# Kernel optimization log

Hardware: AMD Instinct MI355X
Metric: run time of the kernel (lower is better)

## Reference

```python
import jax, jax.numpy as jnp
import numpy as np

D_MODEL = 1024
N_HEADS = 16
HEAD_DIM = 64
T = 4096
ROT = HEAD_DIM // 2          # 32 channels get rotary
PAIR = ROT // 2              # 16 cos/sin frequencies
EPS = 1e-6
SCALE = 0.12                 # constant attention scale (not 1/sqrt(d))
ROPE_BASE = 10000.0
VOCAB = 50257


def setup_inputs() -> dict:
    key = jax.random.key(0)
    k_x, k_qkv, k_o, k_tok = jax.random.split(key, 4)
    bound = 0.5 / np.sqrt(D_MODEL)
    x = jax.random.normal(k_x, (1, T, D_MODEL), dtype=jnp.float32)
    w_qkv = jax.random.uniform(k_qkv, (3 * D_MODEL, D_MODEL), jnp.float32, -bound, bound)
    # module uses zero_init for w_o; use small random so output is non-trivial
    w_o = jax.random.uniform(k_o, (D_MODEL, D_MODEL), jnp.float32, -bound, bound)
    q_norm_w = jnp.ones((HEAD_DIM,), jnp.float32)
    k_norm_w = jnp.ones((HEAD_DIM,), jnp.float32)
    tokens = jax.random.randint(k_tok, (1, T), 0, VOCAB, dtype=jnp.int64)
    pos = jnp.arange(T, dtype=jnp.int64)
    # RotaryCache: inv_freq over pair dims, cos/sin of t * inv_freq
    inv_freq = 1.0 / (ROPE_BASE ** (jnp.arange(PAIR, dtype=jnp.float32) / PAIR))
    freqs = jnp.arange(T, dtype=jnp.float32)[:, None] * inv_freq[None, :]  # [T, PAIR]
    return {
        "x": x, "tokens": tokens, "pos": pos,
        "w_qkv": w_qkv, "w_o": w_o,
        "q_norm_w": q_norm_w, "k_norm_w": k_norm_w,
        "cos": jnp.cos(freqs), "sin": jnp.sin(freqs),
        "window_tokens": 1024, "block_size": 128,
    }


def _rmsnorm(x, w):
    var = jnp.mean(x * x, axis=-1, keepdims=True)
    return x * jax.lax.rsqrt(var + EPS) * w


def reference(x, tokens, pos, w_qkv, w_o, q_norm_w, k_norm_w, cos, sin,
              window_tokens, block_size):
    B, Tq, C = x.shape
    H, Dh = N_HEADS, HEAD_DIM
    qkv = x @ w_qkv.T                                  # [B, T, 3C]
    q, k, v = jnp.split(qkv, 3, axis=-1)

    def to_bhtd(t):
        return t.reshape(B, Tq, H, Dh).transpose(0, 2, 1, 3)
    q, k, v = to_bhtd(q), to_bhtd(k), to_bhtd(v)

    q = _rmsnorm(q, q_norm_w)
    k = _rmsnorm(k, k_norm_w)

    # half-truncated RoPE: rotate first ROT channels pairwise (even/odd)
    c = cos[pos][None, None]                           # [1,1,T,PAIR]
    s = sin[pos][None, None]

    def rope_rotate(t):
        t1, t2 = t[..., :ROT], t[..., ROT:]
        even, odd = t1[..., 0::2], t1[..., 1::2]
        r_even = even * c - odd * s
        r_odd = even * s + odd * c
        t1r = jnp.stack([r_even, r_odd], axis=-1).reshape(t1.shape)
        return jnp.concatenate([t1r, t2], axis=-1)

    q = rope_rotate(q)
    k = rope_rotate(k)

    v = v * 0.5                                        # no value-embed branch

    scores = jnp.einsum('bhtd,bhsd->bhts', q, k) * SCALE
    idx = jnp.arange(Tq)
    diff = idx[:, None] - idx[None, :]
    allowed = (diff >= 0) & (diff < window_tokens)     # sliding causal window
    scores = jnp.where(allowed, scores, -jnp.inf)
    p = jax.nn.softmax(scores, axis=-1)
    out = jnp.einsum('bhts,bhsd->bhtd', p, v)
    out = out.transpose(0, 2, 1, 3).reshape(B, Tq, C)
    return out @ w_o.T
```

## Files before the change

### kernel.cpp

```cpp
#include <hip/hip_runtime.h>


typedef __bf16 bf16x8 __attribute__((ext_vector_type(8)));
typedef __bf16 bf16x2 __attribute__((ext_vector_type(2)));
typedef float f32x4 __attribute__((ext_vector_type(4)));
typedef unsigned short u16x8 __attribute__((ext_vector_type(8)));
typedef unsigned short u16x4 __attribute__((ext_vector_type(4)));

#define MFMA16(a, b, c) __builtin_amdgcn_mfma_f32_16x16x32_bf16((a), (b), (c), 0, 0, 0)

__device__ __forceinline__ unsigned short f2bf(float f) {
    unsigned int u = __float_as_uint(f);
    u += 0x7fffu + ((u >> 16) & 1u);
    return (unsigned short)(u >> 16);
}
__device__ __forceinline__ float bf2f(unsigned short h) {
    return __uint_as_float(((unsigned int)h) << 16);
}
__device__ __forceinline__ unsigned int pk2bf(float a, float b) {
#if __has_builtin(__builtin_amdgcn_cvt_pk_bf16_f32)
    bf16x2 v = __builtin_amdgcn_cvt_pk_bf16_f32(a, b);
    return __builtin_bit_cast(unsigned int, v);
#else
    return (unsigned int)f2bf(a) | ((unsigned int)f2bf(b) << 16);
#endif
}
__device__ __forceinline__ float fexp2(float x) {
#if __has_builtin(__builtin_amdgcn_exp2f)
    return __builtin_amdgcn_exp2f(x);
#else
    return exp2f(x);
#endif
}

__device__ __forceinline__ void gl_lds16(const void* g, void* l) {
    typedef __attribute__((address_space(1))) unsigned int GU;
    typedef __attribute__((address_space(3))) unsigned int LU;
    __builtin_amdgcn_global_load_lds((GU*)(unsigned long long)g,
                                     (LU*)(unsigned int)(unsigned long long)l,
                                     16, 0, 0);
}

__global__ void cvt3_kernel(const float* __restrict__ x,
                            const float* __restrict__ wqkv,
                            const float* __restrict__ wo,
                            unsigned short* __restrict__ xb,
                            unsigned short* __restrict__ wqkvb,
                            unsigned short* __restrict__ wob) {
    int i = blockIdx.x * 256 + threadIdx.x;
    const float* src;
    unsigned short* dst;
    int off;
    if (i < 1048576) { src = x; dst = xb; off = i; }
    else if (i < 1835008) { src = wqkv; dst = wqkvb; off = i - 1048576; }
    else { src = wo; dst = wob; off = i - 1835008; }
    float4 f = ((const float4*)src)[off];
    u16x4 o;
    o[0] = f2bf(f.x); o[1] = f2bf(f.y); o[2] = f2bf(f.z); o[3] = f2bf(f.w);
    ((u16x4*)dst)[off] = o;
}

#define TBS 72
__global__ __launch_bounds__(256, 6) void gemm_qkv(
    const unsigned short* __restrict__ A,
    const unsigned short* __restrict__ Bt,
    const float* __restrict__ cosb, const float* __restrict__ sinb,
    const float* __restrict__ qw, const float* __restrict__ kw,
    unsigned short* __restrict__ Qb,
    unsigned short* __restrict__ Kb,
    unsigned short* __restrict__ Vt)
{
    __shared__ unsigned short smem[12288];
    unsigned short* As0 = smem;
    unsigned short* As1 = smem + 2048;
    unsigned short* Bs0 = smem + 4096;
    unsigned short* Bs1 = smem + 8192;

    const int tid = threadIdx.x;
    const int wave = tid >> 6, lane = tid & 63;
    const int quad = lane >> 4, l16 = lane & 15;
    const int m0 = blockIdx.x * 64, n0 = blockIdx.y * 128;
    const int wm = (wave >> 1) * 32, wn = (wave & 1) * 64;

    f32x4 acc[2][4];
#pragma unroll
    for (int i = 0; i < 2; ++i)
#pragma unroll
        for (int j = 0; j < 4; ++j) acc[i][j] = (f32x4){0.f, 0.f, 0.f, 0.f};

    const int lrow = lane >> 2, lcol = (lane & 3) * 8;

    for (int k0 = 0; k0 < 1024; k0 += 64) {
        {
            const unsigned short* ab = A + (size_t)(m0 + wave * 16 + lrow) * 1024 + k0 + lcol;
            gl_lds16(ab,      &As0[wave * 512]);
            gl_lds16(ab + 32, &As1[wave * 512]);
        }
#pragma unroll
        for (int i = 0; i < 2; ++i) {
            const int c = wave * 2 + i;
            const unsigned short* bb = Bt + (size_t)(n0 + c * 16 + lrow) * 1024 + k0 + lcol;
            gl_lds16(bb,      &Bs0[c * 512]);
            gl_lds16(bb + 32, &Bs1[c * 512]);
        }
        __syncthreads();
        {
            bf16x8 af[2], bfr[4];
#pragma unroll
            for (int mt = 0; mt < 2; ++mt)
                af[mt] = *(const bf16x8*)&As0[(wm + mt * 16 + l16) * 32 + quad * 8];
#pragma unroll
            for (int nt = 0; nt < 4; ++nt)
                bfr[nt] = *(const bf16x8*)&Bs0[(wn + nt * 16 + l16) * 32 + quad * 8];
#pragma unroll
            for (int mt = 0; mt < 2; ++mt)
#pragma unroll
                for (int nt = 0; nt < 4; ++nt)
                    acc[mt][nt] = MFMA16(af[mt], bfr[nt], acc[mt][nt]);
        }
        {
            bf16x8 af[2], bfr[4];
#pragma unroll
            for (int mt = 0; mt < 2; ++mt)
                af[mt] = *(const bf16x8*)&As1[(wm + mt * 16 + l16) * 32 + quad * 8];
#pragma unroll
            for (int nt = 0; nt < 4; ++nt)
                bfr[nt] = *(const bf16x8*)&Bs1[(wn + nt * 16 + l16) * 32 + quad * 8];
#pragma unroll
            for (int mt = 0; mt < 2; ++mt)
#pragma unroll
                for (int nt = 0; nt < 4; ++nt)
                    acc[mt][nt] = MFMA16(af[mt], bfr[nt], acc[mt][nt]);
        }
        __syncthreads();
    }

    unsigned short* tbw = smem + wave * 1152;
    const int region = blockIdx.y >> 3;
    const int h = ((blockIdx.y & 7) << 1) + (wave & 1);

    if (region < 2) {
        const float* wgt = region ? kw : qw;
        unsigned short* dst = region ? Kb : Qb;
        const float post = region ? 1.f : 0.17312340490667046f;
        float w[4];
#pragma unroll
        for (int nt = 0; nt < 4; ++nt) w[nt] = wgt[nt * 16 + l16] * post;
#pragma unroll
        for (int mt = 0; mt < 2; ++mt) {
#pragma unroll
            for (int r = 0; r < 4; ++r) {
                const int row = m0 + wm + mt * 16 + quad * 4 + r;
                float ss = 0.f;
#pragma unroll
                for (int nt = 0; nt < 4; ++nt)
                    ss += acc[mt][nt][r] * acc[mt][nt][r];
                ss += __shfl_xor(ss, 1); ss += __shfl_xor(ss, 2);
                ss += __shfl_xor(ss, 4); ss += __shfl_xor(ss, 8);
                const float rn = rsqrtf(ss * (1.f / 64.f) + 1e-6f);
                float val[4];
#pragma unroll
                for (int nt = 0; nt < 4; ++nt)
                    val[nt] = acc[mt][nt][r] * rn * w[nt];
#pragma unroll
                for (int nt = 0; nt < 2; ++nt) {
                    const float prt = __shfl_xor(val[nt], 1);
                    const int p = nt * 8 + (l16 >> 1);
                    const float c = cosb[row * 16 + p];
                    const float s = sinb[row * 16 + p];
                    val[nt] = (l16 & 1) ? (prt * s + val[nt] * c)
                                        : (val[nt] * c - prt * s);
                }
#pragma unroll
                for (int nt = 0; nt < 4; ++nt)
                    tbw[(quad * 4 + r) * TBS + nt * 16 + l16] = f2bf(val[nt]);
            }
            const int t = lane >> 2, dcol = (lane & 3) * 16;
            u16x8 v0 = *(const u16x8*)&tbw[t * TBS + dcol];
            u16x8 v1 = *(const u16x8*)&tbw[t * TBS + dcol + 8];
            const size_t ob = ((size_t)h * 4096 + (m0 + wm + mt * 16 + t)) * 64 + dcol;
            *(u16x8*)&dst[ob] = v0;
            *(u16x8*)&dst[ob + 8] = v1;
        }
    } else {
#pragma unroll
        for (int mt = 0; mt < 2; ++mt) {
#pragma unroll
            for (int nt = 0; nt < 4; ++nt)
#pragma unroll
                for (int r = 0; r < 4; ++r)
                    tbw[(nt * 16 + l16) * 16 + quad * 4 + r] =
                        f2bf(acc[mt][nt][r] * 0.5f);
            u16x8 v0 = *(const u16x8*)&tbw[lane * 16];
            u16x8 v1 = *(const u16x8*)&tbw[lane * 16 + 8];
            const size_t vo = ((size_t)h * 64 + lane) * 4096 + m0 + wm + mt * 16;
            *(u16x8*)&Vt[vo] = v0;
            *(u16x8*)&Vt[vo + 8] = v1;
        }
    }
}

#define PSTR 72

template <int MODE>
__device__ __forceinline__ void attn_step(
    int s0, int tq, int wave, int quad, int l16, int krow, int kcol,
    const unsigned short* __restrict__ Kh, const unsigned short* __restrict__ Vh,
    unsigned short* Ks0, unsigned short* Ks1,
    unsigned short* Vs0, unsigned short* Vs1, unsigned short* Pw,
    const bf16x8 qf0, const bf16x8 qf1, f32x4 (&o)[4], float& lsum)
{
    __syncthreads();
    const unsigned short* kb = Kh + (size_t)(s0 + krow) * 64 + kcol;
    const unsigned short* vb = Vh + (size_t)krow * 4096 + s0 + kcol;
    gl_lds16(kb,      &Ks0[wave * 512]);
    gl_lds16(kb + 32, &Ks1[wave * 512]);
    gl_lds16(vb,      &Vs0[wave * 512]);
    gl_lds16(vb + 32, &Vs1[wave * 512]);
    __syncthreads();

#pragma unroll
    for (int i = 0; i < 4; ++i) {
        const bf16x8 kf0 = *(const bf16x8*)&Ks0[(i * 16 + l16) * 32 + quad * 8];
        const bf16x8 kf1 = *(const bf16x8*)&Ks1[(i * 16 + l16) * 32 + quad * 8];
        f32x4 z = (f32x4){0.f, 0.f, 0.f, 0.f};
        z = MFMA16(kf0, qf0, z);
        z = MFMA16(kf1, qf1, z);
        float p[4];
#pragma unroll
        for (int r = 0; r < 4; ++r) {
            float e = fexp2(z[r]);
            if (MODE == 1) {
                const int s = s0 + i * 16 + quad * 4 + r;
                e = ((tq - s) < 1024) ? e : 0.f;
            }
            if (MODE == 2) {
                const int s = s0 + i * 16 + quad * 4 + r;
                e = (s <= tq) ? e : 0.f;
            }
            p[r] = e;
            lsum += e;
        }
        uint2 pk;
        pk.x = pk2bf(p[0], p[1]);
        pk.y = pk2bf(p[2], p[3]);
        *(uint2*)&Pw[l16 * PSTR + i * 16 + quad * 4] = pk;
    }
    const bf16x8 pf0 = *(const bf16x8*)&Pw[l16 * PSTR + quad * 8];
    const bf16x8 pf1 = *(const bf16x8*)&Pw[l16 * PSTR + 32 + quad * 8];
#pragma unroll
    for (int dt = 0; dt < 4; ++dt) {
        const bf16x8 vf0 = *(const bf16x8*)&Vs0[(dt * 16 + l16) * 32 + quad * 8];
        const bf16x8 vf1 = *(const bf16x8*)&Vs1[(dt * 16 + l16) * 32 + quad * 8];
        o[dt] = MFMA16(pf0, vf0, o[dt]);
        o[dt] = MFMA16(pf1, vf1, o[dt]);
    }
}

__global__ __launch_bounds__(256) void attn_kernel(
    const unsigned short* __restrict__ Qb,
    const unsigned short* __restrict__ Kb,
    const unsigned short* __restrict__ Vt,
    unsigned short* __restrict__ att)
{
    __shared__ unsigned short Ks0[64 * 32];
    __shared__ unsigned short Ks1[64 * 32];
    __shared__ unsigned short Vs0[64 * 32];
    __shared__ unsigned short Vs1[64 * 32];
    __shared__ unsigned short P[4][16 * PSTR];

    const int bid = blockIdx.x;
    const int h = ((bid & 7) << 1) | ((bid >> 3) & 1);
    const int t0 = (63 - (bid >> 4)) * 64;

    const int tid = threadIdx.x;
    const int wave = tid >> 6, lane = tid & 63;
    const int quad = lane >> 4, l16 = lane & 15;
    const int qt0 = t0 + wave * 16;
    const int tq = qt0 + l16;
    const int krow = tid >> 2, kcol = (tid & 3) * 8;

    const unsigned short* Qh = Qb + (size_t)h * 4096 * 64;
    const unsigned short* Kh = Kb + (size_t)h * 4096 * 64;
    const unsigned short* Vh = Vt + (size_t)h * 64 * 4096;

    const bf16x8 qf0 = *(const bf16x8*)&Qh[(qt0 + l16) * 64 + quad * 8];
    const bf16x8 qf1 = *(const bf16x8*)&Qh[(qt0 + l16) * 64 + 32 + quad * 8];

    f32x4 o[4];
#pragma unroll
    for (int dt = 0; dt < 4; ++dt) o[dt] = (f32x4){0.f, 0.f, 0.f, 0.f};
    float lsum = 0.f;
    unsigned short* Pw = P[wave];

    int s0 = (t0 >= 1024) ? (t0 - 1024) : 0;
    if (t0 >= 1024) {
        attn_step<1>(s0, tq, wave, quad, l16, krow, kcol, Kh, Vh,
                     Ks0, Ks1, Vs0, Vs1, Pw, qf0, qf1, o, lsum);
        s0 += 64;
    }
    for (; s0 < t0; s0 += 64)
        attn_step<0>(s0, tq, wave, quad, l16, krow, kcol, Kh, Vh,
                     Ks0, Ks1, Vs0, Vs1, Pw, qf0, qf1, o, lsum);
    attn_step<2>(t0, tq, wave, quad, l16, krow, kcol, Kh, Vh,
                 Ks0, Ks1, Vs0, Vs1, Pw, qf0, qf1, o, lsum);

    lsum += __shfl_xor(lsum, 16);
    lsum += __shfl_xor(lsum, 32);
    float lr[4];
#pragma unroll
    for (int r = 0; r < 4; ++r) lr[r] = 1.f / __shfl(lsum, quad * 4 + r);
#pragma unroll
    for (int dt = 0; dt < 4; ++dt)
#pragma unroll
        for (int r = 0; r < 4; ++r)
            att[(size_t)(qt0 + quad * 4 + r) * 1024 + h * 64 + dt * 16 + l16] =
                f2bf(o[dt][r] * lr[r]);
}

template <int BM, bool F32OUT>
__global__ __launch_bounds__(256) void gemm_bt(
    const unsigned short* __restrict__ A,
    const unsigned short* __restrict__ Bt,
    void* __restrict__ Cp, int N, int K) {
    __shared__ unsigned short As[2][BM * 32];
    __shared__ unsigned short Bs[2][128 * 32];
    constexpr int MT = BM / 32;
    const int tid = threadIdx.x;
    const int wave = tid >> 6, lane = tid & 63;
    const int quad = lane >> 4, l16 = lane & 15;
    const int m0 = blockIdx.x * BM, n0 = blockIdx.y * 128;
    const int wm = (wave >> 1) * (BM / 2), wn = (wave & 1) * 64;

    f32x4 acc[MT][4];
#pragma unroll
    for (int i = 0; i < MT; ++i)
#pragma unroll
        for (int j = 0; j < 4; ++j) acc[i][j] = (f32x4){0.f, 0.f, 0.f, 0.f};

    auto stageAB = [&](int buf, int k0) {
#pragma unroll
        for (int i = 0; i < BM / 64; ++i) {
            const int c = wave * (BM / 64) + i;
            const int e = (c * 64 + lane) * 8;
            const int r = e >> 5, col = e & 31;
            gl_lds16(A + (size_t)(m0 + r) * K + (k0 + col), &As[buf][c * 512]);
        }
#pragma unroll
        for (int i = 0; i < 2; ++i) {
            const int c = wave * 2 + i;
            const int e = (c * 64 + lane) * 8;
            const int r = e >> 5, col = e & 31;
            gl_lds16(Bt + (size_t)(n0 + r) * K + (k0 + col), &Bs[buf][c * 512]);
        }
    };

    stageAB(0, 0);
    __syncthreads();
    int buf = 0;
    for (int k0 = 0; k0 < K; k0 += 32) {
        if (k0 + 32 < K) stageAB(buf ^ 1, k0 + 32);
        bf16x8 af[MT], bfr[4];
#pragma unroll
        for (int mt = 0; mt < MT; ++mt)
            af[mt] = *(const bf16x8*)&As[buf][(wm + mt * 16 + l16) * 32 + quad * 8];
#pragma unroll
        for (int nt = 0; nt < 4; ++nt)
            bfr[nt] = *(const bf16x8*)&Bs[buf][(wn + nt * 16 + l16) * 32 + quad * 8];
#pragma unroll
        for (int mt = 0; mt < MT; ++mt)
#pragma unroll
            for (int nt = 0; nt < 4; ++nt)
                acc[mt][nt] = MFMA16(af[mt], bfr[nt], acc[mt][nt]);
        __syncthreads();
        buf ^= 1;
    }
#pragma unroll
    for (int mt = 0; mt < MT; ++mt)
#pragma unroll
        for (int nt = 0; nt < 4; ++nt)
#pragma unroll
            for (int r = 0; r < 4; ++r) {
                const int row = m0 + wm + mt * 16 + quad * 4 + r;
                const int col = n0 + wn + nt * 16 + l16;
                const float v = acc[mt][nt][r];
                if (F32OUT)
                    ((float*)Cp)[(size_t)row * N + col] = v;
                else
                    ((unsigned short*)Cp)[(size_t)row * N + col] = f2bf(v);
            }
}

extern "C" void kernel_launch(void* const* d_in, const int* in_sizes, int n_in,
                              void* d_out, int out_size, void* d_ws, size_t ws_size,
                              hipStream_t stream) {
    const float* x    = (const float*)d_in[0];
    const float* wqkv = (const float*)d_in[3];
    const float* wo   = (const float*)d_in[4];
    const float* qw   = (const float*)d_in[5];
    const float* kw   = (const float*)d_in[6];
    const float* cosb = (const float*)d_in[7];
    const float* sinb = (const float*)d_in[8];

    char* ws = (char*)d_ws;
    if (ws_size < (size_t)48 * 1024 * 1024) return;
    unsigned short* xb    = (unsigned short*)(ws + ((size_t)0 << 20));
    unsigned short* wqkvb = (unsigned short*)(ws + ((size_t)8 << 20));
    unsigned short* wob   = (unsigned short*)(ws + ((size_t)14 << 20));
    unsigned short* Qb    = (unsigned short*)(ws + ((size_t)16 << 20));
    unsigned short* Kb    = (unsigned short*)(ws + ((size_t)24 << 20));
    unsigned short* Vt    = (unsigned short*)(ws + ((size_t)32 << 20));
    unsigned short* attb  = (unsigned short*)(ws + ((size_t)40 << 20));

    cvt3_kernel<<<8192, 256, 0, stream>>>(x, wqkv, wo, xb, wqkvb, wob);

    gemm_qkv<<<dim3(64, 24), 256, 0, stream>>>(xb, wqkvb, cosb, sinb, qw, kw,
                                               Qb, Kb, Vt);

    attn_kernel<<<1024, 256, 0, stream>>>(Qb, Kb, Vt, attb);

    gemm_bt<64, true><<<dim3(64, 8), 256, 0, stream>>>(attb, wob, (float*)d_out, 1024, 1024);
}
```

Measured before the change: 188.0 us.

## Restructure attention into single-wave blocks reading K/V directly from global

```diff
diff --git a/kernel.cpp b/kernel.cpp
--- a/kernel.cpp
+++ b/kernel.cpp
@@ -204,118 +204,137 @@
 
 template <int MODE>
 __device__ __forceinline__ void attn_step(
-    int s0, int tq, int wave, int quad, int l16, int krow, int kcol,
+    int s0, int tqA, int tqB, int quad, int l16,
     const unsigned short* __restrict__ Kh, const unsigned short* __restrict__ Vh,
-    unsigned short* Ks0, unsigned short* Ks1,
-    unsigned short* Vs0, unsigned short* Vs1, unsigned short* Pw,
-    const bf16x8 qf0, const bf16x8 qf1, f32x4 (&o)[4], float& lsum)
+    unsigned short* PA, unsigned short* PB,
+    const bf16x8 qfA0, const bf16x8 qfA1,
+    const bf16x8 qfB0, const bf16x8 qfB1,
+    f32x4 (&oA)[4], f32x4 (&oB)[4], float& lsA, float& lsB)
 {
-    __syncthreads();
-    const unsigned short* kb = Kh + (size_t)(s0 + krow) * 64 + kcol;
-    const unsigned short* vb = Vh + (size_t)krow * 4096 + s0 + kcol;
-    gl_lds16(kb,      &Ks0[wave * 512]);
-    gl_lds16(kb + 32, &Ks1[wave * 512]);
-    gl_lds16(vb,      &Vs0[wave * 512]);
-    gl_lds16(vb + 32, &Vs1[wave * 512]);
-    __syncthreads();
-
-#pragma unroll
-    for (int i = 0; i < 4; ++i) {
-        const bf16x8 kf0 = *(const bf16x8*)&Ks0[(i * 16 + l16) * 32 + quad * 8];
-        const bf16x8 kf1 = *(const bf16x8*)&Ks1[(i * 16 + l16) * 32 + quad * 8];
-        f32x4 z = (f32x4){0.f, 0.f, 0.f, 0.f};
-        z = MFMA16(kf0, qf0, z);
-        z = MFMA16(kf1, qf1, z);
-        float p[4];
+    constexpr int NSUB = (MODE == 3) ? 2 : 4;
+#pragma unroll
+    for (int i = 0; i < NSUB; ++i) {
+        const unsigned short* kr = &Kh[(size_t)(s0 + i * 16 + l16) * 64 + quad * 8];
+        const bf16x8 kf0 = *(const bf16x8*)kr;
+        const bf16x8 kf1 = *(const bf16x8*)(kr + 32);
+        f32x4 zA = (f32x4){0.f, 0.f, 0.f, 0.f};
+        f32x4 zB = (f32x4){0.f, 0.f, 0.f, 0.f};
+        zA = MFMA16(kf0, qfA0, zA); zA = MFMA16(kf1, qfA1, zA);
+        zB = MFMA16(kf0, qfB0, zB); zB = MFMA16(kf1, qfB1, zB);
+        float pA[4], pB[4];
 #pragma unroll
         for (int r = 0; r < 4; ++r) {
-            float e = fexp2(z[r]);
+            const int s = s0 + i * 16 + quad * 4 + r;
+            float eA = fexp2(zA[r]);
+            float eB = fexp2(zB[r]);
             if (MODE == 1) {
-                const int s = s0 + i * 16 + quad * 4 + r;
-                e = ((tq - s) < 1024) ? e : 0.f;
+                eA = ((tqA - s) < 1024) ? eA : 0.f;
+                eB = ((tqB - s) < 1024) ? eB : 0.f;
             }
-            if (MODE == 2) {
-                const int s = s0 + i * 16 + quad * 4 + r;
-                e = (s <= tq) ? e : 0.f;
+            if (MODE == 2 || MODE == 3) {
+                eA = (s <= tqA) ? eA : 0.f;
+                eB = (s <= tqB) ? eB : 0.f;
             }
-            p[r] = e;
-            lsum += e;
-        }
-        uint2 pk;
-        pk.x = pk2bf(p[0], p[1]);
-        pk.y = pk2bf(p[2], p[3]);
-        *(uint2*)&Pw[l16 * PSTR + i * 16 + quad * 4] = pk;
-    }
-    const bf16x8 pf0 = *(const bf16x8*)&Pw[l16 * PSTR + quad * 8];
-    const bf16x8 pf1 = *(const bf16x8*)&Pw[l16 * PSTR + 32 + quad * 8];
+            pA[r] = eA; pB[r] = eB;
+            lsA += eA; lsB += eB;
+        }
+        uint2 wa, wb;
+        wa.x = pk2bf(pA[0], pA[1]); wa.y = pk2bf(pA[2], pA[3]);
+        wb.x = pk2bf(pB[0], pB[1]); wb.y = pk2bf(pB[2], pB[3]);
+        *(uint2*)&PA[l16 * PSTR + i * 16 + quad * 4] = wa;
+        *(uint2*)&PB[l16 * PSTR + i * 16 + quad * 4] = wb;
+    }
+    const bf16x8 pA0 = *(const bf16x8*)&PA[l16 * PSTR + quad * 8];
+    const bf16x8 pB0 = *(const bf16x8*)&PB[l16 * PSTR + quad * 8];
+    bf16x8 pA1, pB1;
+    if (MODE != 3) {
+        pA1 = *(const bf16x8*)&PA[l16 * PSTR + 32 + quad * 8];
+        pB1 = *(const bf16x8*)&PB[l16 * PSTR + 32 + quad * 8];
+    }
 #pragma unroll
     for (int dt = 0; dt < 4; ++dt) {
-        const bf16x8 vf0 = *(const bf16x8*)&Vs0[(dt * 16 + l16) * 32 + quad * 8];
-        const bf16x8 vf1 = *(const bf16x8*)&Vs1[(dt * 16 + l16) * 32 + quad * 8];
-        o[dt] = MFMA16(pf0, vf0, o[dt]);
-        o[dt] = MFMA16(pf1, vf1, o[dt]);
-    }
-}
-
-__global__ __launch_bounds__(256) void attn_kernel(
+        const unsigned short* vr = &Vh[(size_t)(dt * 16 + l16) * 4096 + s0 + quad * 8];
+        const bf16x8 vf0 = *(const bf16x8*)vr;
+        oA[dt] = MFMA16(pA0, vf0, oA[dt]);
+        oB[dt] = MFMA16(pB0, vf0, oB[dt]);
+        if (MODE != 3) {
+            const bf16x8 vf1 = *(const bf16x8*)(vr + 32);
+            oA[dt] = MFMA16(pA1, vf1, oA[dt]);
+            oB[dt] = MFMA16(pB1, vf1, oB[dt]);
+        }
+    }
+}
+
+__global__ __launch_bounds__(64) void attn_kernel(
     const unsigned short* __restrict__ Qb,
     const unsigned short* __restrict__ Kb,
     const unsigned short* __restrict__ Vt,
     unsigned short* __restrict__ att)
 {
-    __shared__ unsigned short Ks0[64 * 32];
-    __shared__ unsigned short Ks1[64 * 32];
-    __shared__ unsigned short Vs0[64 * 32];
-    __shared__ unsigned short Vs1[64 * 32];
-    __shared__ unsigned short P[4][16 * PSTR];
+    __shared__ unsigned short P[2][16 * PSTR];
 
     const int bid = blockIdx.x;
     const int h = ((bid & 7) << 1) | ((bid >> 3) & 1);
-    const int t0 = (63 - (bid >> 4)) * 64;
-
-    const int tid = threadIdx.x;
-    const int wave = tid >> 6, lane = tid & 63;
+    const int t0 = (127 - (bid >> 4)) * 32;
+
+    const int lane = threadIdx.x;
     const int quad = lane >> 4, l16 = lane & 15;
-    const int qt0 = t0 + wave * 16;
-    const int tq = qt0 + l16;
-    const int krow = tid >> 2, kcol = (tid & 3) * 8;
+    const int tqA = t0 + l16, tqB = t0 + 16 + l16;
 
     const unsigned short* Qh = Qb + (size_t)h * 4096 * 64;
     const unsigned short* Kh = Kb + (size_t)h * 4096 * 64;
     const unsigned short* Vh = Vt + (size_t)h * 64 * 4096;
 
-    const bf16x8 qf0 = *(const bf16x8*)&Qh[(qt0 + l16) * 64 + quad * 8];
-    const bf16x8 qf1 = *(const bf16x8*)&Qh[(qt0 + l16) * 64 + 32 + quad * 8];
-
-    f32x4 o[4];
-#pragma unroll
-    for (int dt = 0; dt < 4; ++dt) o[dt] = (f32x4){0.f, 0.f, 0.f, 0.f};
-    float lsum = 0.f;
-    unsigned short* Pw = P[wave];
-
-    int s0 = (t0 >= 1024) ? (t0 - 1024) : 0;
+    const bf16x8 qfA0 = *(const bf16x8*)&Qh[(t0 + l16) * 64 + quad * 8];
+    const bf16x8 qfA1 = *(const bf16x8*)&Qh[(t0 + l16) * 64 + 32 + quad * 8];
+    const bf16x8 qfB0 = *(const bf16x8*)&Qh[(t0 + 16 + l16) * 64 + quad * 8];
+    const bf16x8 qfB1 = *(const bf16x8*)&Qh[(t0 + 16 + l16) * 64 + 32 + quad * 8];
+
+    f32x4 oA[4], oB[4];
+#pragma unroll
+    for (int dt = 0; dt < 4; ++dt) {
+        oA[dt] = (f32x4){0.f, 0.f, 0.f, 0.f};
+        oB[dt] = (f32x4){0.f, 0.f, 0.f, 0.f};
+    }
+    float lsA = 0.f, lsB = 0.f;
+    unsigned short* PA = P[0];
+    unsigned short* PB = P[1];
+
+    const int sb = (t0 >= 1024) ? ((t0 - 1023) & ~63) : 0;
+    const int sd = t0 & ~63;
+    int s0 = sb;
     if (t0 >= 1024) {
-        attn_step<1>(s0, tq, wave, quad, l16, krow, kcol, Kh, Vh,
-                     Ks0, Ks1, Vs0, Vs1, Pw, qf0, qf1, o, lsum);
+        attn_step<1>(s0, tqA, tqB, quad, l16, Kh, Vh, PA, PB,
+                     qfA0, qfA1, qfB0, qfB1, oA, oB, lsA, lsB);
         s0 += 64;
     }
-    for (; s0 < t0; s0 += 64)
-        attn_step<0>(s0, tq, wave, quad, l16, krow, kcol, Kh, Vh,
-                     Ks0, Ks1, Vs0, Vs1, Pw, qf0, qf1, o, lsum);
-    attn_step<2>(t0, tq, wave, quad, l16, krow, kcol, Kh, Vh,
-                 Ks0, Ks1, Vs0, Vs1, Pw, qf0, qf1, o, lsum);
-
-    lsum += __shfl_xor(lsum, 16);
-    lsum += __shfl_xor(lsum, 32);
-    float lr[4];
-#pragma unroll
-    for (int r = 0; r < 4; ++r) lr[r] = 1.f / __shfl(lsum, quad * 4 + r);
+    for (; s0 < sd; s0 += 64)
+        attn_step<0>(s0, tqA, tqB, quad, l16, Kh, Vh, PA, PB,
+                     qfA0, qfA1, qfB0, qfB1, oA, oB, lsA, lsB);
+    if (t0 & 32)
+        attn_step<2>(sd, tqA, tqB, quad, l16, Kh, Vh, PA, PB,
+                     qfA0, qfA1, qfB0, qfB1, oA, oB, lsA, lsB);
+    else
+        attn_step<3>(sd, tqA, tqB, quad, l16, Kh, Vh, PA, PB,
+                     qfA0, qfA1, qfB0, qfB1, oA, oB, lsA, lsB);
+
+    lsA += __shfl_xor(lsA, 16); lsA += __shfl_xor(lsA, 32);
+    lsB += __shfl_xor(lsB, 16); lsB += __shfl_xor(lsB, 32);
+    float lrA[4], lrB[4];
+#pragma unroll
+    for (int r = 0; r < 4; ++r) {
+        lrA[r] = 1.f / __shfl(lsA, quad * 4 + r);
+        lrB[r] = 1.f / __shfl(lsB, quad * 4 + r);
+    }
 #pragma unroll
     for (int dt = 0; dt < 4; ++dt)
 #pragma unroll
-        for (int r = 0; r < 4; ++r)
-            att[(size_t)(qt0 + quad * 4 + r) * 1024 + h * 64 + dt * 16 + l16] =
-                f2bf(o[dt][r] * lr[r]);
+        for (int r = 0; r < 4; ++r) {
+            att[(size_t)(t0 + quad * 4 + r) * 1024 + h * 64 + dt * 16 + l16] =
+                f2bf(oA[dt][r] * lrA[r]);
+            att[(size_t)(t0 + 16 + quad * 4 + r) * 1024 + h * 64 + dt * 16 + l16] =
+                f2bf(oB[dt][r] * lrB[r]);
+        }
 }
 
 template <int BM, bool F32OUT>
@@ -417,7 +436,7 @@
     gemm_qkv<<<dim3(64, 24), 256, 0, stream>>>(xb, wqkvb, cosb, sinb, qw, kw,
                                                Qb, Kb, Vt);
 
-    attn_kernel<<<1024, 256, 0, stream>>>(Qb, Kb, Vt, attb);
+    attn_kernel<<<2048, 64, 0, stream>>>(Qb, Kb, Vt, attb);
 
     gemm_bt<64, true><<<dim3(64, 8), 256, 0, stream>>>(attb, wob, (float*)d_out, 1024, 1024);
 }
```

New measurement: 219.1 us. 1.17x slower.

## Read V fragments directly from global and widen output GEMM K-step

Applied to the files above, without the earlier changes.

```diff
diff --git a/kernel.cpp b/kernel.cpp
--- a/kernel.cpp
+++ b/kernel.cpp
@@ -206,17 +206,13 @@
 __device__ __forceinline__ void attn_step(
     int s0, int tq, int wave, int quad, int l16, int krow, int kcol,
     const unsigned short* __restrict__ Kh, const unsigned short* __restrict__ Vh,
-    unsigned short* Ks0, unsigned short* Ks1,
-    unsigned short* Vs0, unsigned short* Vs1, unsigned short* Pw,
+    unsigned short* Ks0, unsigned short* Ks1, unsigned short* Pw,
     const bf16x8 qf0, const bf16x8 qf1, f32x4 (&o)[4], float& lsum)
 {
     __syncthreads();
     const unsigned short* kb = Kh + (size_t)(s0 + krow) * 64 + kcol;
-    const unsigned short* vb = Vh + (size_t)krow * 4096 + s0 + kcol;
     gl_lds16(kb,      &Ks0[wave * 512]);
     gl_lds16(kb + 32, &Ks1[wave * 512]);
-    gl_lds16(vb,      &Vs0[wave * 512]);
-    gl_lds16(vb + 32, &Vs1[wave * 512]);
     __syncthreads();
 
 #pragma unroll
@@ -250,8 +246,9 @@
     const bf16x8 pf1 = *(const bf16x8*)&Pw[l16 * PSTR + 32 + quad * 8];
 #pragma unroll
     for (int dt = 0; dt < 4; ++dt) {
-        const bf16x8 vf0 = *(const bf16x8*)&Vs0[(dt * 16 + l16) * 32 + quad * 8];
-        const bf16x8 vf1 = *(const bf16x8*)&Vs1[(dt * 16 + l16) * 32 + quad * 8];
+        const unsigned short* vr = &Vh[(size_t)(dt * 16 + l16) * 4096 + s0 + quad * 8];
+        const bf16x8 vf0 = *(const bf16x8*)vr;
+        const bf16x8 vf1 = *(const bf16x8*)(vr + 32);
         o[dt] = MFMA16(pf0, vf0, o[dt]);
         o[dt] = MFMA16(pf1, vf1, o[dt]);
     }
@@ -265,8 +262,6 @@
 {
     __shared__ unsigned short Ks0[64 * 32];
     __shared__ unsigned short Ks1[64 * 32];
-    __shared__ unsigned short Vs0[64 * 32];
-    __shared__ unsigned short Vs1[64 * 32];
     __shared__ unsigned short P[4][16 * PSTR];
 
     const int bid = blockIdx.x;
@@ -296,14 +291,14 @@
     int s0 = (t0 >= 1024) ? (t0 - 1024) : 0;
     if (t0 >= 1024) {
         attn_step<1>(s0, tq, wave, quad, l16, krow, kcol, Kh, Vh,
-                     Ks0, Ks1, Vs0, Vs1, Pw, qf0, qf1, o, lsum);
+                     Ks0, Ks1, Pw, qf0, qf1, o, lsum);
         s0 += 64;
     }
     for (; s0 < t0; s0 += 64)
         attn_step<0>(s0, tq, wave, quad, l16, krow, kcol, Kh, Vh,
-                     Ks0, Ks1, Vs0, Vs1, Pw, qf0, qf1, o, lsum);
+                     Ks0, Ks1, Pw, qf0, qf1, o, lsum);
     attn_step<2>(t0, tq, wave, quad, l16, krow, kcol, Kh, Vh,
-                 Ks0, Ks1, Vs0, Vs1, Pw, qf0, qf1, o, lsum);
+                 Ks0, Ks1, Pw, qf0, qf1, o, lsum);
 
     lsum += __shfl_xor(lsum, 16);
     lsum += __shfl_xor(lsum, 32);
@@ -318,76 +313,84 @@
                 f2bf(o[dt][r] * lr[r]);
 }
 
-template <int BM, bool F32OUT>
-__global__ __launch_bounds__(256) void gemm_bt(
+__global__ __launch_bounds__(256) void gemm_out(
     const unsigned short* __restrict__ A,
     const unsigned short* __restrict__ Bt,
-    void* __restrict__ Cp, int N, int K) {
-    __shared__ unsigned short As[2][BM * 32];
-    __shared__ unsigned short Bs[2][128 * 32];
-    constexpr int MT = BM / 32;
+    float* __restrict__ C)
+{
+    __shared__ unsigned short As0[2][2048], As1[2][2048];
+    __shared__ unsigned short Bs0[2][4096], Bs1[2][4096];
     const int tid = threadIdx.x;
     const int wave = tid >> 6, lane = tid & 63;
     const int quad = lane >> 4, l16 = lane & 15;
-    const int m0 = blockIdx.x * BM, n0 = blockIdx.y * 128;
-    const int wm = (wave >> 1) * (BM / 2), wn = (wave & 1) * 64;
-
-    f32x4 acc[MT][4];
-#pragma unroll
-    for (int i = 0; i < MT; ++i)
+    const int m0 = blockIdx.x * 64, n0 = blockIdx.y * 128;
+    const int wm = (wave >> 1) * 32, wn = (wave & 1) * 64;
+    const int lrow = lane >> 2, lcol = (lane & 3) * 8;
+
+    f32x4 acc[2][4];
+#pragma unroll
+    for (int i = 0; i < 2; ++i)
 #pragma unroll
         for (int j = 0; j < 4; ++j) acc[i][j] = (f32x4){0.f, 0.f, 0.f, 0.f};
 
-    auto stageAB = [&](int buf, int k0) {
-#pragma unroll
-        for (int i = 0; i < BM / 64; ++i) {
-            const int c = wave * (BM / 64) + i;
-            const int e = (c * 64 + lane) * 8;
-            const int r = e >> 5, col = e & 31;
-            gl_lds16(A + (size_t)(m0 + r) * K + (k0 + col), &As[buf][c * 512]);
-        }
+    auto stage = [&](int buf, int k0) {
+        const unsigned short* ab = A + (size_t)(m0 + wave * 16 + lrow) * 1024 + k0 + lcol;
+        gl_lds16(ab,      &As0[buf][wave * 512]);
+        gl_lds16(ab + 32, &As1[buf][wave * 512]);
 #pragma unroll
         for (int i = 0; i < 2; ++i) {
             const int c = wave * 2 + i;
-            const int e = (c * 64 + lane) * 8;
-            const int r = e >> 5, col = e & 31;
-            gl_lds16(Bt + (size_t)(n0 + r) * K + (k0 + col), &Bs[buf][c * 512]);
+            const unsigned short* bb = Bt + (size_t)(n0 + c * 16 + lrow) * 1024 + k0 + lcol;
+            gl_lds16(bb,      &Bs0[buf][c * 512]);
+            gl_lds16(bb + 32, &Bs1[buf][c * 512]);
         }
     };
 
-    stageAB(0, 0);
+    stage(0, 0);
     __syncthreads();
     int buf = 0;
-    for (int k0 = 0; k0 < K; k0 += 32) {
-        if (k0 + 32 < K) stageAB(buf ^ 1, k0 + 32);
-        bf16x8 af[MT], bfr[4];
-#pragma unroll
-        for (int mt = 0; mt < MT; ++mt)
-            af[mt] = *(const bf16x8*)&As[buf][(wm + mt * 16 + l16) * 32 + quad * 8];
-#pragma unroll
-        for (int nt = 0; nt < 4; ++nt)
-            bfr[nt] = *(const bf16x8*)&Bs[buf][(wn + nt * 16 + l16) * 32 + quad * 8];
-#pragma unroll
-        for (int mt = 0; mt < MT; ++mt)
+    for (int k0 = 0; k0 < 1024; k0 += 64) {
+        if (k0 + 64 < 1024) stage(buf ^ 1, k0 + 64);
+        {
+            bf16x8 af[2], bfr[4];
+#pragma unroll
+            for (int mt = 0; mt < 2; ++mt)
+                af[mt] = *(const bf16x8*)&As0[buf][(wm + mt * 16 + l16) * 32 + quad * 8];
 #pragma unroll
             for (int nt = 0; nt < 4; ++nt)
-                acc[mt][nt] = MFMA16(af[mt], bfr[nt], acc[mt][nt]);
+                bfr[nt] = *(const bf16x8*)&Bs0[buf][(wn + nt * 16 + l16) * 32 + quad * 8];
+#pragma unroll
+            for (int mt = 0; mt < 2; ++mt)
+#pragma unroll
+                for (int nt = 0; nt < 4; ++nt)
+                    acc[mt][nt] = MFMA16(af[mt], bfr[nt], acc[mt][nt]);
+        }
+        {
+            bf16x8 af[2], bfr[4];
+#pragma unroll
+            for (int mt = 0; mt < 2; ++mt)
+                af[mt] = *(const bf16x8*)&As1[buf][(wm + mt * 16 + l16) * 32 + quad * 8];
+#pragma unroll
+            for (int nt = 0; nt < 4; ++nt)
+                bfr[nt] = *(const bf16x8*)&Bs1[buf][(wn + nt * 16 + l16) * 32 + quad * 8];
+#pragma unroll
+            for (int mt = 0; mt < 2; ++mt)
+#pragma unroll
+                for (int nt = 0; nt < 4; ++nt)
+                    acc[mt][nt] = MFMA16(af[mt], bfr[nt], acc[mt][nt]);
+        }
         __syncthreads();
         buf ^= 1;
     }
 #pragma unroll
-    for (int mt = 0; mt < MT; ++mt)
+    for (int mt = 0; mt < 2; ++mt)
 #pragma unroll
         for (int nt = 0; nt < 4; ++nt)
 #pragma unroll
             for (int r = 0; r < 4; ++r) {
                 const int row = m0 + wm + mt * 16 + quad * 4 + r;
                 const int col = n0 + wn + nt * 16 + l16;
-                const float v = acc[mt][nt][r];
-                if (F32OUT)
-                    ((float*)Cp)[(size_t)row * N + col] = v;
-                else
-                    ((unsigned short*)Cp)[(size_t)row * N + col] = f2bf(v);
+                C[(size_t)row * 1024 + col] = acc[mt][nt][r];
             }
 }
 
@@ -419,5 +422,5 @@
 
     attn_kernel<<<1024, 256, 0, stream>>>(Qb, Kb, Vt, attb);
 
-    gemm_bt<64, true><<<dim3(64, 8), 256, 0, stream>>>(attb, wob, (float*)d_out, 1024, 1024);
-}
+    gemm_out<<<dim3(64, 8), 256, 0, stream>>>(attb, wob, (float*)d_out);
+}
```

Measured after the change: 214.8 us. 1.14x slower.
